# Optimization experiments

Hardware: AMD Instinct MI355X
Metric: run time of the kernel (lower is better)

## Reference

```python
import jax, jax.numpy as jnp
import numpy as np
from jax import lax

MAX_INT = 10000.0
V, T0, E, H = 100000, 20, 256, 256
T = T0 + 2          # tagset_size + 2 (start = T-2, stop = T-1)
B, S = 32, 512
H2 = H // 2


def setup_inputs() -> dict:
    key = jax.random.key(0)
    ks = jax.random.split(key, 18)
    sd = 0.08
    trans = jax.random.normal(ks[0], (T, T), jnp.float32)
    trans = trans.at[-2, :].set(-MAX_INT).at[:, -1].set(-MAX_INT)
    return {
        "X": jax.random.randint(ks[1], (B, S), 0, V, jnp.int64),
        "Y": jax.random.randint(ks[2], (B, S), 0, T0, jnp.int64),
        "emb": jax.random.normal(ks[3], (V, E), jnp.float32) * sd,
        "Wih_f": jax.random.normal(ks[4], (4 * H2, E), jnp.float32) * sd,
        "Whh_f": jax.random.normal(ks[5], (4 * H2, H2), jnp.float32) * sd,
        "bih_f": jax.random.normal(ks[6], (4 * H2,), jnp.float32) * sd,
        "bhh_f": jax.random.normal(ks[7], (4 * H2,), jnp.float32) * sd,
        "Wih_b": jax.random.normal(ks[8], (4 * H2, E), jnp.float32) * sd,
        "Whh_b": jax.random.normal(ks[9], (4 * H2, H2), jnp.float32) * sd,
        "bih_b": jax.random.normal(ks[10], (4 * H2,), jnp.float32) * sd,
        "bhh_b": jax.random.normal(ks[11], (4 * H2,), jnp.float32) * sd,
        "fcW": jax.random.normal(ks[12], (T, H), jnp.float32) * sd,
        "fcb": jax.random.normal(ks[13], (T,), jnp.float32) * sd,
        "trans": trans,
        # original draws random (h0, c0) of shape (2, seq_len, H//2) each call
        "h0": jax.random.normal(ks[14], (2, S, H2), jnp.float32),
        "c0": jax.random.normal(ks[15], (2, S, H2), jnp.float32),
    }


def _lstm_dir(x, h0, c0, Wih, Whh, bih, bhh, reverse):
    # x: [B, S, E]; scans over axis 0 (as torch LSTM with batch_first=False does here)
    def step(carry, xt):
        h, c = carry
        g = xt @ Wih.T + bih + h @ Whh.T + bhh          # [S, 4*H2]
        i, f, gg, o = jnp.split(g, 4, axis=-1)
        c2 = jax.nn.sigmoid(f) * c + jax.nn.sigmoid(i) * jnp.tanh(gg)
        h2 = jax.nn.sigmoid(o) * jnp.tanh(c2)
        return (h2, c2), h2
    xs = x[::-1] if reverse else x
    _, hs = lax.scan(step, (h0, c0), xs)
    return hs[::-1] if reverse else hs                  # [B, S, H2]


def _feats(X, emb, Wih_f, Whh_f, bih_f, bhh_f, Wih_b, Whh_b, bih_b, bhh_b,
           fcW, fcb, h0, c0):
    e = emb[X]                                           # [B, S, E]
    hf = _lstm_dir(e, h0[0], c0[0], Wih_f, Whh_f, bih_f, bhh_f, False)
    hb = _lstm_dir(e, h0[1], c0[1], Wih_b, Whh_b, bih_b, bhh_b, True)
    lstm_out = jnp.concatenate([hf, hb], axis=-1)        # [B, S, H]
    return lstm_out @ fcW.T + fcb                        # [B, S, T]


def _crf_loss(feats, Y, trans):
    # forward algorithm (log partition), vectorized over batch
    alpha0 = jnp.full((B, T), -MAX_INT, feats.dtype).at[:, -2].set(0.0)

    def step(alpha, feat_t):                             # feat_t: [B, T]
        # alpha_new[b, next] = LSE_prev(alpha[b,prev] + trans[next,prev]) + feat[b,next]
        new = jax.nn.logsumexp(alpha[:, None, :] + trans[None, :, :], axis=2) + feat_t
        return new, None

    alpha, _ = lax.scan(step, alpha0, jnp.swapaxes(feats, 0, 1))
    forward_score = jax.nn.logsumexp(alpha + trans[-1][None, :], axis=1).mean()

    # gold score
    start = jnp.full((B, 1), T - 2, Y.dtype)
    tags = jnp.concatenate([start, Y], axis=1)           # [B, S+1]
    emit = jnp.take_along_axis(feats, Y[..., None], axis=2)[..., 0].sum(axis=1)
    trans_sc = trans[tags[:, 1:], tags[:, :-1]].sum(axis=1) + trans[-1, tags[:, -1]]
    gold_score = (emit + trans_sc).mean()
    return forward_score - gold_score


def reference(X, Y, emb, Wih_f, Whh_f, bih_f, bhh_f, Wih_b, Whh_b, bih_b, bhh_b,
              fcW, fcb, trans, h0, c0):
    feats = _feats(X, emb, Wih_f, Whh_f, bih_f, bhh_f, Wih_b, Whh_b, bih_b, bhh_b,
                   fcW, fcb, h0, c0)
    score = _crf_loss(feats, Y, trans)
    return score, Y
```

## Files before the change

### kernel.cpp

```cpp
#include <hip/hip_runtime.h>
#include <hip/hip_bf16.h>
#include <stdint.h>

typedef __attribute__((ext_vector_type(8))) short short8;
typedef __attribute__((ext_vector_type(4))) float f32x4;
typedef __attribute__((ext_vector_type(4))) unsigned short ushort4v;

#define NB 32
#define NS 512
#define NE 256
#define NH2 128
#define NG 512
#define NT 22

__device__ __forceinline__ unsigned short f2bf(float f) {
    union { float f; unsigned u; } v; v.f = f;
    unsigned r = v.u + 0x7fffu + ((v.u >> 16) & 1u);
    return (unsigned short)(r >> 16);
}
__device__ __forceinline__ float bf2f(unsigned short b) {
    union { unsigned u; float f; } v; v.u = ((unsigned)b) << 16;
    return v.f;
}
__device__ __forceinline__ float sigmoidf_(float x) {
    return __builtin_amdgcn_rcpf(1.f + __expf(-x));
}
__device__ __forceinline__ float tanhf_(float x) {
    return 1.f - 2.f * __builtin_amdgcn_rcpf(__expf(2.f * x) + 1.f);
}
__device__ __forceinline__ void wg_barrier() {
    __builtin_amdgcn_sched_barrier(0);
    asm volatile("s_waitcnt lgkmcnt(0)" ::: "memory");
    __builtin_amdgcn_s_barrier();
    __builtin_amdgcn_sched_barrier(0);
}
#define GL16(gsrc, ldst)                                                              \
    __builtin_amdgcn_global_load_lds(                                                 \
        (const __attribute__((address_space(1))) unsigned int*)(gsrc),                \
        (__attribute__((address_space(3))) unsigned int*)(ldst), 16, 0, 0)

__global__ void k_pre(const int* X, const float* emb, const int* Y,
                      const float* Wih_f, const float* Wih_b,
                      const float* Whh_f, const float* Whh_b, const float* fcW,
                      unsigned short* ebf, unsigned short* Wb_ih,
                      unsigned short* Wb_hh, unsigned short* fcpad, float* out)
{
    int idx = blockIdx.x * blockDim.x + threadIdx.x;
    const int nEmb = NB * NS * 64;
    if (idx < nEmb) {
        int r = idx >> 6, lane = idx & 63;
        int xr = X[r];
        f32x4 v = *(const f32x4*)(emb + (size_t)xr * NE + lane * 4);
        ushort4v o;
        o[0] = f2bf(v[0]); o[1] = f2bf(v[1]); o[2] = f2bf(v[2]); o[3] = f2bf(v[3]);
        *(ushort4v*)(ebf + (size_t)r * NE + lane * 4) = o;
        return;
    }
    int j = idx - nEmb;
    const int n1 = 2 * NG * NE;
    const int n2 = 2 * NG * NH2;
    const int n3 = 2 * 32 * NH2;
    const int n4 = NB * NS;
    if (j < n1) {
        const float* src = (j < NG * NE) ? Wih_f : Wih_b;
        Wb_ih[j] = f2bf(src[j % (NG * NE)]);
    } else if (j < n1 + n2) {
        int i2 = j - n1;
        const float* src = (i2 < NG * NH2) ? Whh_f : Whh_b;
        Wb_hh[i2] = f2bf(src[i2 % (NG * NH2)]);
    } else if (j < n1 + n2 + n3) {
        int i3 = j - n1 - n2;
        int d = i3 / (32 * NH2);
        int jj = (i3 / NH2) % 32;
        int k = i3 % NH2;
        fcpad[i3] = (jj < NT) ? f2bf(fcW[jj * 256 + d * NH2 + k]) : (unsigned short)0;
    } else if (j < n1 + n2 + n3 + n4) {
        int i4 = j - n1 - n2 - n3;
        out[1 + i4] = (float)Y[i4];
    }
}

__launch_bounds__(256)
__global__ void k_xproj(const unsigned short* ebf, const unsigned short* Wb_ih,
                        const float* bih_f, const float* bhh_f,
                        const float* bih_b, const float* bhh_b,
                        unsigned short* Xp)
{
    __shared__ __align__(16) unsigned short Atile[2][128 * 64];
    __shared__ __align__(16) unsigned short Btile[2][128 * 64];
    int dir = blockIdx.z;
    int r0 = blockIdx.x * 128;
    int g0 = blockIdx.y * 128;
    int tid = threadIdx.x;
    int w = tid >> 6, lane = tid & 63;
    int wr = w >> 1, wc = w & 1;
    int lrow = lane & 15, kg = lane >> 4;
    int srow8 = lane >> 3, schunk = lane & 7;
    const float* bih = dir ? bih_b : bih_f;
    const float* bhh = dir ? bhh_b : bhh_f;
    const unsigned short* Bsrc = Wb_ih + ((size_t)dir * NG + g0) * NE;
    const unsigned short* Asrc = ebf + (size_t)r0 * NE;

#define STAGE(bufi, ks)                                                                \
    do {                                                                               \
        int k0_ = (ks) * 64;                                                           \
        _Pragma("unroll")                                                              \
        for (int i_ = 0; i_ < 4; ++i_) {                                               \
            int rr_ = (w * 4 + i_) * 8 + srow8;                                        \
            GL16(Asrc + (size_t)rr_ * NE + k0_ + schunk * 8, &Atile[bufi][(w * 4 + i_) * 512]); \
            GL16(Bsrc + (size_t)rr_ * NE + k0_ + schunk * 8, &Btile[bufi][(w * 4 + i_) * 512]); \
        }                                                                              \
    } while (0)

    STAGE(0, 0);
    f32x4 acc[4][4] = {};
#pragma unroll
    for (int ks = 0; ks < 4; ++ks) {
        const int cur = ks & 1;
        if (ks < 3) {
            STAGE(cur ^ 1, ks + 1);
            asm volatile("s_waitcnt vmcnt(8)" ::: "memory");
        } else {
            asm volatile("s_waitcnt vmcnt(0)" ::: "memory");
        }
        __builtin_amdgcn_sched_barrier(0);
        __builtin_amdgcn_s_barrier();
        __builtin_amdgcn_sched_barrier(0);
        short8 a[4][2], b[4][2];
#pragma unroll
        for (int mi = 0; mi < 4; ++mi)
#pragma unroll
            for (int kk = 0; kk < 2; ++kk)
                a[mi][kk] = *(const short8*)&Atile[cur][(wr * 64 + mi * 16 + lrow) * 64 + kk * 32 + kg * 8];
#pragma unroll
        for (int ni = 0; ni < 4; ++ni)
#pragma unroll
            for (int kk = 0; kk < 2; ++kk)
                b[ni][kk] = *(const short8*)&Btile[cur][(wc * 64 + ni * 16 + lrow) * 64 + kk * 32 + kg * 8];
#pragma unroll
        for (int mi = 0; mi < 4; ++mi)
#pragma unroll
            for (int ni = 0; ni < 4; ++ni)
#pragma unroll
                for (int kk = 0; kk < 2; ++kk)
                    acc[mi][ni] = __builtin_amdgcn_mfma_f32_16x16x32_bf16(a[mi][kk], b[ni][kk], acc[mi][ni], 0, 0, 0);
        asm volatile("s_waitcnt lgkmcnt(0)" ::: "memory");
        __builtin_amdgcn_sched_barrier(0);
        __builtin_amdgcn_s_barrier();
        __builtin_amdgcn_sched_barrier(0);
    }
#undef STAGE

#pragma unroll
    for (int ni = 0; ni < 4; ++ni) {
        int g = g0 + wc * 64 + ni * 16 + lrow;
        float bias = bih[g] + bhh[g];
#pragma unroll
        for (int mi = 0; mi < 4; ++mi) {
            int r = r0 + wr * 64 + mi * 16 + kg * 4;
            int t = r >> 9;
            int s = r & 511;
            int sb = s >> 4;
            unsigned short* dst = Xp + ((((size_t)dir * 32 + sb) * 32 + t) << 13) + g * 16 + (s & 15);
            unsigned o0 = f2bf(acc[mi][ni][0] + bias);
            unsigned o1 = f2bf(acc[mi][ni][1] + bias);
            unsigned o2 = f2bf(acc[mi][ni][2] + bias);
            unsigned o3 = f2bf(acc[mi][ni][3] + bias);
            uint2 pk; pk.x = o0 | (o1 << 16); pk.y = o2 | (o3 << 16);
            *(uint2*)dst = pk;
        }
    }
}

__launch_bounds__(512, 2)
__global__ void k_lstm(const unsigned short* Wb_hh, const unsigned short* fcpad,
                       const unsigned short* Xp, const float* h0, const float* c0,
                       float* featsP)
{
    __shared__ unsigned short h_lds[2][16 * 136];
    __shared__ float featsL[32 * 16 * 24];
    int dir = blockIdx.x >> 5;
    int sb = blockIdx.x & 31;
    int s0 = sb * 16;
    int tid = threadIdx.x;
    int w = tid >> 6, lane = tid & 63;
    int lrow = lane & 15, kg = lane >> 4;

    short8 bfr[4][4];
#pragma unroll
    for (int q = 0; q < 4; ++q) {
        const unsigned short* p = Wb_hh + ((size_t)dir * NG + (q * 128 + w * 16 + lrow)) * NH2 + kg * 8;
#pragma unroll
        for (int kf = 0; kf < 4; ++kf)
            bfr[q][kf] = *(const short8*)(p + kf * 32);
    }
    short8 fcfr[4];
    if (w < 2) {
        const unsigned short* p = fcpad + ((size_t)dir * 32 + (w * 16 + lrow)) * NH2 + kg * 8;
#pragma unroll
        for (int kf = 0; kf < 4; ++kf)
            fcfr[kf] = *(const short8*)(p + kf * 32);
    }

    float c[4];
#pragma unroll
    for (int i = 0; i < 4; ++i)
        c[i] = c0[((size_t)dir * NS + s0 + kg * 4 + i) * NH2 + w * 16 + lrow];
    {
        int sl = tid >> 5, hq = tid & 31;
        f32x4 hv = *(const f32x4*)(h0 + ((size_t)dir * NS + s0 + sl) * NH2 + hq * 4);
        ushort4v hb; hb[0] = f2bf(hv[0]); hb[1] = f2bf(hv[1]); hb[2] = f2bf(hv[2]); hb[3] = f2bf(hv[3]);
        *(ushort4v*)&h_lds[0][sl * 136 + hq * 4] = hb;
    }

    const unsigned short* xbase = Xp + (((size_t)dir * 32 + sb) * 32) * 8192;
    int xoff0 = (w * 16 + lrow) * 16 + kg * 4;
    ushort4v xA[4], xB[4];
#pragma unroll
    for (int q = 0; q < 4; ++q)
        xA[q] = *(const ushort4v*)(xbase + (size_t)(dir ? 31 : 0) * 8192 + xoff0 + q * 2048);
#pragma unroll
    for (int q = 0; q < 4; ++q)
        xB[q] = *(const ushort4v*)(xbase + (size_t)(dir ? 30 : 1) * 8192 + xoff0 + q * 2048);
    __syncthreads();

#define LSTM_STEP(T, XV, PR, PW)                                                       \
    {                                                                                  \
        short8 afr[4];                                                                 \
        _Pragma("unroll")                                                              \
        for (int kf = 0; kf < 4; ++kf)                                                 \
            afr[kf] = *(const short8*)&h_lds[PR][lrow * 136 + kf * 32 + kg * 8];       \
        f32x4 acc[4] = {};                                                             \
        _Pragma("unroll")                                                              \
        for (int q = 0; q < 4; ++q)                                                    \
            _Pragma("unroll")                                                          \
            for (int kf = 0; kf < 4; ++kf)                                             \
                acc[q] = __builtin_amdgcn_mfma_f32_16x16x32_bf16(afr[kf], bfr[q][kf],  \
                                                                 acc[q], 0, 0, 0);     \
        if (w < 2 && (T) > 0) {                     \
            int txp = dir ? 32 - (T) : (T) - 1;                                        \
            f32x4 fa = {};                                                             \
            _Pragma("unroll")                                                          \
            for (int kf = 0; kf < 4; ++kf)                                             \
                fa = __builtin_amdgcn_mfma_f32_16x16x32_bf16(afr[kf], fcfr[kf], fa, 0, 0, 0); \
            int tag = w * 16 + lrow;                                                   \
            if (tag < NT) {                                                            \
                _Pragma("unroll")                                                      \
                for (int i = 0; i < 4; ++i)                                            \
                    featsL[(txp * 16 + kg * 4 + i) * 24 + tag] = fa[i];                \
            }                                                                          \
        }                                                                              \
        float gs[4][4];                                                                \
        _Pragma("unroll")                                                              \
        for (int q = 0; q < 4; ++q)                                                    \
            _Pragma("unroll")                                                          \
            for (int i = 0; i < 4; ++i)                                                \
                gs[q][i] = acc[q][i] + bf2f(XV[q][i]);                                 \
        if ((T) + 2 < 32) {                                                            \
            int txn = dir ? 29 - (T) : (T) + 2;                                        \
            _Pragma("unroll")                                                          \
            for (int q = 0; q < 4; ++q)                                                \
                XV[q] = *(const ushort4v*)(xbase + (size_t)txn * 8192 + xoff0 + q * 2048); \
        }                                                                              \
        _Pragma("unroll")                                                              \
        for (int i = 0; i < 4; ++i) {                                                  \
            float ci = sigmoidf_(gs[1][i]) * c[i] + sigmoidf_(gs[0][i]) * tanhf_(gs[2][i]); \
            c[i] = ci;                                                                 \
            h_lds[PW][(kg * 4 + i) * 136 + w * 16 + lrow] = f2bf(sigmoidf_(gs[3][i]) * tanhf_(ci)); \
        }                                                                              \
        wg_barrier();                                                                  \
    }

    for (int tt = 0; tt < 16; ++tt) {
        LSTM_STEP(2 * tt,     xA, ((2 * tt) & 1),     (((2 * tt) & 1) ^ 1))
        LSTM_STEP(2 * tt + 1, xB, ((2 * tt + 1) & 1), (((2 * tt + 1) & 1) ^ 1))
    }
#undef LSTM_STEP

    if (w < 2) {
        short8 afr[4];
#pragma unroll
        for (int kf = 0; kf < 4; ++kf)
            afr[kf] = *(const short8*)&h_lds[0][lrow * 136 + kf * 32 + kg * 8];
        f32x4 fa = {};
#pragma unroll
        for (int kf = 0; kf < 4; ++kf)
            fa = __builtin_amdgcn_mfma_f32_16x16x32_bf16(afr[kf], fcfr[kf], fa, 0, 0, 0);
        int txl = dir ? 0 : 31;
        int tag = w * 16 + lrow;
        if (tag < NT) {
#pragma unroll
            for (int i = 0; i < 4; ++i)
                featsL[(txl * 16 + kg * 4 + i) * 24 + tag] = fa[i];
        }
    }
    __syncthreads();
    int ftx = tid >> 4, fs = tid & 15;
    float* gdst = featsP + (((size_t)dir * 32 + ftx) * 512 + s0 + fs) * 24;
    const float* lsrc = featsL + (ftx * 16 + fs) * 24;
#pragma unroll
    for (int j = 0; j < 6; ++j)
        ((f32x4*)gdst)[j] = ((const f32x4*)lsrc)[j];
}

__device__ __forceinline__ float mm_combine(const unsigned short* Rb, const unsigned short* Tb,
                                            int lane, f32x4 c[2][2])
{
    int lrow = lane & 15, kg = lane >> 4;
    short8 a0 = *(const short8*)(Rb + lrow * 32 + kg * 8);
    short8 a1 = *(const short8*)(Rb + (16 + lrow) * 32 + kg * 8);
    short8 b0 = *(const short8*)(Tb + lrow * 32 + kg * 8);
    short8 b1 = *(const short8*)(Tb + (16 + lrow) * 32 + kg * 8);
    c[0][0] = __builtin_amdgcn_mfma_f32_16x16x32_bf16(a0, b0, c[0][0], 0, 0, 0);
    c[0][1] = __builtin_amdgcn_mfma_f32_16x16x32_bf16(a0, b1, c[0][1], 0, 0, 0);
    c[1][0] = __builtin_amdgcn_mfma_f32_16x16x32_bf16(a1, b0, c[1][0], 0, 0, 0);
    c[1][1] = __builtin_amdgcn_mfma_f32_16x16x32_bf16(a1, b1, c[1][1], 0, 0, 0);
    float mx = 0.f;
#pragma unroll
    for (int ti = 0; ti < 2; ++ti)
#pragma unroll
        for (int tj = 0; tj < 2; ++tj)
#pragma unroll
            for (int i = 0; i < 4; ++i) mx = fmaxf(mx, c[ti][tj][i]);
#pragma unroll
    for (int off = 32; off; off >>= 1) mx = fmaxf(mx, __shfl_xor(mx, off));
    return fmaxf(mx, 1e-30f);
}

__device__ __forceinline__ void write_scaled(unsigned short* outp, bool Rlayout,
                                             int lane, const f32x4 c[2][2], float inv)
{
    int lrow = lane & 15, kg = lane >> 4;
    if (Rlayout) {
#pragma unroll
        for (int ti = 0; ti < 2; ++ti)
#pragma unroll
            for (int tj = 0; tj < 2; ++tj) {
                int cc = tj * 16 + lrow;
#pragma unroll
                for (int i = 0; i < 4; ++i) {
                    int r = ti * 16 + kg * 4 + i;
                    float v = (r < NT && cc < NT) ? c[ti][tj][i] * inv : 0.f;
                    outp[r * 32 + cc] = f2bf(v);
                }
            }
    } else {
#pragma unroll
        for (int ti = 0; ti < 2; ++ti)
#pragma unroll
            for (int tj = 0; tj < 2; ++tj) {
                int cc = tj * 16 + lrow;
                int r0 = ti * 16 + kg * 4;
                ushort4v pk;
#pragma unroll
                for (int i = 0; i < 4; ++i) {
                    int r = r0 + i;
                    float v = (r < NT && cc < NT) ? c[ti][tj][i] * inv : 0.f;
                    pk[i] = f2bf(v);
                }
                *(ushort4v*)(outp + cc * 32 + r0) = pk;
            }
    }
}

__launch_bounds__(256)
__global__ void k_fcrf(const float* featsP, const float* fcb, const float* trans,
                       const int* Y, unsigned short* Mseg, float* lscseg, float* goldp)
{
    __shared__ unsigned short mats[16 * 1024];
    __shared__ float etR[484], etT[484];
    __shared__ float ef[16 * 24];
    __shared__ float fl[16 * 24];
    __shared__ float lscm[16];
    int b = blockIdx.x, seg = blockIdx.y;
    int tid = threadIdx.x;
    int w = tid >> 6, lane = tid & 63;

    for (int i = tid; i < 484; i += 256) {
        float e = __expf(trans[i]);
        etR[i] = e;
        etT[(i % NT) * NT + (i / NT)] = e;
    }
    for (int i = tid; i < 16 * NT; i += 256) {
        int s = i / NT, j = i % NT;
        size_t base = ((size_t)b * 512 + seg * 16 + s) * 24 + j;
        float f = featsP[base] + featsP[(size_t)32 * 512 * 24 + base] + fcb[j];
        fl[s * 24 + j] = f;
        ef[s * 24 + j] = __expf(f);
    }
    if (tid < 16) lscm[tid] = 0.f;
    __syncthreads();

    if (w == 3 && lane < 16) {
        int sg = seg * 16 + lane;
        int y = Y[b * NS + sg];
        int yp = sg ? Y[b * NS + sg - 1] : (NT - 2);
        float gp = fl[lane * 24 + y] + trans[y * NT + yp];
#pragma unroll
        for (int off = 8; off; off >>= 1) gp += __shfl_xor(gp, off);
        if (lane == 0) goldp[b * 32 + seg] = gp;
    }

    for (int idx = tid; idx < 16 * 1024; idx += 256) {
        int t = idx >> 10, cell = idx & 1023, row = cell >> 5, col = cell & 31;
        float v = 0.f;
        if (row < NT && col < NT) {
            v = (t & 1) ? etR[row * NT + col] * ef[t * 24 + row]
                        : etT[row * NT + col] * ef[t * 24 + col];
        }
        mats[idx] = f2bf(v);
    }
    __syncthreads();

    for (int lvl = 0; lvl < 4; ++lvl) {
        int nP = 8 >> lvl;
        for (int p = w; p < nP; p += 4) {
            int aslot = (2 * p) << lvl, bslot = (2 * p + 1) << lvl;
            f32x4 c[2][2] = {};
            float mx = mm_combine(mats + bslot * 1024, mats + aslot * 1024, lane, c);
            float inv = __builtin_amdgcn_rcpf(mx);
            float nlsc = lscm[aslot] + lscm[bslot] + __logf(mx);
            if (lvl < 3) {
                write_scaled(mats + aslot * 1024, (p & 1) != 0, lane, c, inv);
                if (lane == 0) lscm[aslot] = nlsc;
            } else {
                write_scaled(Mseg + ((size_t)b * 32 + seg) * 1024, (seg & 1) != 0, lane, c, inv);
                if (lane == 0) lscseg[b * 32 + seg] = nlsc;
            }
        }
        __syncthreads();
    }
}

__launch_bounds__(256)
__global__ void k_crf2(const unsigned short* Mseg, const float* lscseg,
                       const float* trans, const int* Y, const float* goldp,
                       float* fwd_sc, float* gold_sc)
{
    __shared__ unsigned short mats[16 * 1024];
    __shared__ float lscm[16];
    __shared__ float tl[484];
    __shared__ float col20[32];
    int b = blockIdx.x;
    int tid = threadIdx.x;
    int w = tid >> 6, lane = tid & 63;
    int lrow = lane & 15, kg = lane >> 4;

    for (int i = tid; i < 484; i += 256) tl[i] = trans[i];
    __syncthreads();

    const unsigned short* base = Mseg + (size_t)b * 32 * 1024;
    for (int p = w; p < 16; p += 4) {
        f32x4 c[2][2] = {};
        float mx = mm_combine(base + (2 * p + 1) * 1024, base + (2 * p) * 1024, lane, c);
        float inv = __builtin_amdgcn_rcpf(mx);
        float nlsc = lscseg[b * 32 + 2 * p] + lscseg[b * 32 + 2 * p + 1] + __logf(mx);
        write_scaled(mats + p * 1024, (p & 1) != 0, lane, c, inv);
        if (lane == 0) lscm[p] = nlsc;
    }
    __syncthreads();

    for (int lvl = 0; lvl < 4; ++lvl) {
        int nP = 8 >> lvl;
        for (int p = w; p < nP; p += 4) {
            int aslot = (2 * p) << lvl, bslot = (2 * p + 1) << lvl;
            f32x4 c[2][2] = {};
            float mx = mm_combine(mats + bslot * 1024, mats + aslot * 1024, lane, c);
            if (lvl < 3) {
                float inv = __builtin_amdgcn_rcpf(mx);
                float nlsc = lscm[aslot] + lscm[bslot] + __logf(mx);
                write_scaled(mats + aslot * 1024, (p & 1) != 0, lane, c, inv);
                if (lane == 0) lscm[aslot] = nlsc;
            } else {
                if (lrow == 4) {
#pragma unroll
                    for (int ti = 0; ti < 2; ++ti)
#pragma unroll
                        for (int i = 0; i < 4; ++i)
                            col20[ti * 16 + kg * 4 + i] = c[ti][1][i];
                }
                if (lane == 0) lscm[0] = lscm[0] + lscm[8];
            }
        }
        __syncthreads();
    }

    if (w == 0) {
        float v = 0.f;
        if (lane < NT) v = __expf(tl[(NT - 1) * NT + lane]) * col20[lane];
#pragma unroll
        for (int off = 32; off; off >>= 1) v += __shfl_xor(v, off);
        if (lane == 0) fwd_sc[b] = __logf(v) + lscm[0];
    }
    if (w == 1) {
        float g = (lane < 32) ? goldp[b * 32 + lane] : 0.f;
#pragma unroll
        for (int off = 16; off; off >>= 1) g += __shfl_xor(g, off);
        if (lane == 0) gold_sc[b] = g + tl[(NT - 1) * NT + Y[b * NS + NS - 1]];
    }
}

__global__ void k_final(const float* fwd_sc, const float* gold_sc, float* out)
{
    float v = (threadIdx.x < NB) ? (fwd_sc[threadIdx.x] - gold_sc[threadIdx.x]) : 0.f;
#pragma unroll
    for (int off = 32; off; off >>= 1) v += __shfl_xor(v, off);
    if (threadIdx.x == 0) out[0] = v * (1.f / NB);
}

extern "C" void kernel_launch(void* const* d_in, const int* in_sizes, int n_in,
                              void* d_out, int out_size, void* d_ws, size_t ws_size,
                              hipStream_t stream)
{
    const int* X = (const int*)d_in[0];
    const int* Y = (const int*)d_in[1];
    const float* emb = (const float*)d_in[2];
    const float* Wih_f = (const float*)d_in[3];
    const float* Whh_f = (const float*)d_in[4];
    const float* bih_f = (const float*)d_in[5];
    const float* bhh_f = (const float*)d_in[6];
    const float* Wih_b = (const float*)d_in[7];
    const float* Whh_b = (const float*)d_in[8];
    const float* bih_b = (const float*)d_in[9];
    const float* bhh_b = (const float*)d_in[10];
    const float* fcW = (const float*)d_in[11];
    const float* fcb = (const float*)d_in[12];
    const float* trans = (const float*)d_in[13];
    const float* h0 = (const float*)d_in[14];
    const float* c0 = (const float*)d_in[15];
    float* out = (float*)d_out;

    char* ws = (char*)d_ws;
    unsigned short* Wb_ih = (unsigned short*)(ws + 0);
    unsigned short* Wb_hh = (unsigned short*)(ws + 524288);
    unsigned short* fcpad = (unsigned short*)(ws + 786432);
    unsigned short* Xp    = (unsigned short*)(ws + 802816);
    float* featsP         = (float*)(ws + 34357248);
    float* goldp          = (float*)(ws + 37502976);
    float* fwd_sc         = (float*)(ws + 37507072);
    float* gold_sc        = (float*)(ws + 37507200);
    unsigned short* ebf   = (unsigned short*)(ws + 37507328);
    unsigned short* Mseg  = ebf;
    float* lscseg         = (float*)(ws + 45895936);

    k_pre<<<dim3(5728), dim3(256), 0, stream>>>(X, emb, Y, Wih_f, Wih_b, Whh_f, Whh_b,
                                                fcW, ebf, Wb_ih, Wb_hh, fcpad, out);
    k_xproj<<<dim3(128, 4, 2), dim3(256), 0, stream>>>(ebf, Wb_ih, bih_f, bhh_f, bih_b, bhh_b, Xp);
    k_lstm<<<dim3(64), dim3(512), 0, stream>>>(Wb_hh, fcpad, Xp, h0, c0, featsP);
    k_fcrf<<<dim3(32, 32), dim3(256), 0, stream>>>(featsP, fcb, trans, Y, Mseg, lscseg, goldp);
    k_crf2<<<dim3(NB), dim3(256), 0, stream>>>(Mseg, lscseg, trans, Y, goldp, fwd_sc, gold_sc);
    k_final<<<dim3(1), dim3(64), 0, stream>>>(fwd_sc, gold_sc, out);
    (void)in_sizes; (void)n_in; (void)out_size; (void)ws_size;
}
```

Baseline: 97.98 us.

## Shorten LSTM recurrence critical path and spread FC projection across waves

Restructures the per-step LSTM recurrence. The x-projection now seeds the MFMA accumulator, and the K reduction is split into two independent accumulator chains to cut dependent MFMA latency. The gate math is merged so fewer reciprocals are needed, and h is packed to bf16 with a hardware convert. The FC feature projection is spread across all 8 waves as partial products in LDS and reduced one step late, instead of two waves doing a serial 4-MFMA chain. Features are stored as bf16, which halves the intermediate traffic at some cost in precision.

```diff
diff --git a/kernel.cpp b/kernel.cpp
--- a/kernel.cpp
+++ b/kernel.cpp
@@ -5,6 +5,7 @@
 typedef __attribute__((ext_vector_type(8))) short short8;
 typedef __attribute__((ext_vector_type(4))) float f32x4;
 typedef __attribute__((ext_vector_type(4))) unsigned short ushort4v;
+typedef __attribute__((ext_vector_type(4))) unsigned int uint4v;
 
 #define NB 32
 #define NS 512
@@ -22,11 +23,10 @@
     union { unsigned u; float f; } v; v.u = ((unsigned)b) << 16;
     return v.f;
 }
-__device__ __forceinline__ float sigmoidf_(float x) {
-    return __builtin_amdgcn_rcpf(1.f + __expf(-x));
-}
-__device__ __forceinline__ float tanhf_(float x) {
-    return 1.f - 2.f * __builtin_amdgcn_rcpf(__expf(2.f * x) + 1.f);
+__device__ __forceinline__ unsigned cvt_pk_bf16(float a, float b) {
+    unsigned r;
+    asm("v_cvt_pk_bf16_f32 %0, %1, %2" : "=v"(r) : "v"(a), "v"(b));
+    return r;
 }
 __device__ __forceinline__ void wg_barrier() {
     __builtin_amdgcn_sched_barrier(0);
@@ -175,10 +175,11 @@
 __launch_bounds__(512, 2)
 __global__ void k_lstm(const unsigned short* Wb_hh, const unsigned short* fcpad,
                        const unsigned short* Xp, const float* h0, const float* c0,
-                       float* featsP)
+                       unsigned short* featsP)
 {
     __shared__ unsigned short h_lds[2][16 * 136];
-    __shared__ float featsL[32 * 16 * 24];
+    __shared__ unsigned short featsL[512 * 24];
+    __shared__ f32x4 fcpart[2][8][64];
     int dir = blockIdx.x >> 5;
     int sb = blockIdx.x & 31;
     int s0 = sb * 16;
@@ -194,13 +195,8 @@
         for (int kf = 0; kf < 4; ++kf)
             bfr[q][kf] = *(const short8*)(p + kf * 32);
     }
-    short8 fcfr[4];
-    if (w < 2) {
-        const unsigned short* p = fcpad + ((size_t)dir * 32 + (w * 16 + lrow)) * NH2 + kg * 8;
-#pragma unroll
-        for (int kf = 0; kf < 4; ++kf)
-            fcfr[kf] = *(const short8*)(p + kf * 32);
-    }
+    short8 fcfr8 = *(const short8*)(fcpad + ((size_t)dir * 32 + ((w >> 2) * 16 + lrow)) * NH2 + (w & 3) * 32 + kg * 8);
+    int fctag = (w >> 2) * 16 + lrow;
 
     float c[4];
 #pragma unroll
@@ -224,38 +220,50 @@
         xB[q] = *(const ushort4v*)(xbase + (size_t)(dir ? 30 : 1) * 8192 + xoff0 + q * 2048);
     __syncthreads();
 
+#define FC_REDUCE(par, hstep)                                                          \
+    if (w < 2) {                                                                       \
+        int txp_ = dir ? 31 - (hstep) : (hstep);                                       \
+        f32x4 fa_ = fcpart[par][w * 4 + 0][lane] + fcpart[par][w * 4 + 1][lane]        \
+                  + fcpart[par][w * 4 + 2][lane] + fcpart[par][w * 4 + 3][lane];       \
+        int tag_ = w * 16 + lrow;                                                      \
+        if (tag_ < NT) {                                                               \
+            unsigned r01_ = cvt_pk_bf16(fa_[0], fa_[1]);                               \
+            unsigned r23_ = cvt_pk_bf16(fa_[2], fa_[3]);                               \
+            int rb_ = (txp_ * 16 + kg * 4) * 24 + tag_;                                \
+            featsL[rb_]      = (unsigned short)r01_;                                   \
+            featsL[rb_ + 24] = (unsigned short)(r01_ >> 16);                           \
+            featsL[rb_ + 48] = (unsigned short)r23_;                                   \
+            featsL[rb_ + 72] = (unsigned short)(r23_ >> 16);                           \
+        }                                                                              \
+    }
+
 #define LSTM_STEP(T, XV, PR, PW)                                                       \
     {                                                                                  \
         short8 afr[4];                                                                 \
         _Pragma("unroll")                                                              \
         for (int kf = 0; kf < 4; ++kf)                                                 \
             afr[kf] = *(const short8*)&h_lds[PR][lrow * 136 + kf * 32 + kg * 8];       \
-        f32x4 acc[4] = {};                                                             \
+        f32x4 accA[4], accB[4];                                                        \
         _Pragma("unroll")                                                              \
-        for (int q = 0; q < 4; ++q)                                                    \
-            _Pragma("unroll")                                                          \
-            for (int kf = 0; kf < 4; ++kf)                                             \
-                acc[q] = __builtin_amdgcn_mfma_f32_16x16x32_bf16(afr[kf], bfr[q][kf],  \
-                                                                 acc[q], 0, 0, 0);     \
-        if (w < 2 && (T) > 0) {                     \
-            int txp = dir ? 32 - (T) : (T) - 1;                                        \
-            f32x4 fa = {};                                                             \
-            _Pragma("unroll")                                                          \
-            for (int kf = 0; kf < 4; ++kf)                                             \
-                fa = __builtin_amdgcn_mfma_f32_16x16x32_bf16(afr[kf], fcfr[kf], fa, 0, 0, 0); \
-            int tag = w * 16 + lrow;                                                   \
-            if (tag < NT) {                                                            \
-                _Pragma("unroll")                                                      \
-                for (int i = 0; i < 4; ++i)                                            \
-                    featsL[(txp * 16 + kg * 4 + i) * 24 + tag] = fa[i];                \
-            }                                                                          \
-        }                                                                              \
-        float gs[4][4];                                                                \
+        for (int q = 0; q < 4; ++q) {                                                  \
+            f32x4 ci_;                                                                 \
+            ci_[0] = bf2f(XV[q][0]); ci_[1] = bf2f(XV[q][1]);                          \
+            ci_[2] = bf2f(XV[q][2]); ci_[3] = bf2f(XV[q][3]);                          \
+            accA[q] = __builtin_amdgcn_mfma_f32_16x16x32_bf16(afr[0], bfr[q][0], ci_, 0, 0, 0); \
+            f32x4 z_ = {};                                                             \
+            accB[q] = __builtin_amdgcn_mfma_f32_16x16x32_bf16(afr[2], bfr[q][2], z_, 0, 0, 0);  \
+        }                                                                              \
         _Pragma("unroll")                                                              \
-        for (int q = 0; q < 4; ++q)                                                    \
-            _Pragma("unroll")                                                          \
-            for (int i = 0; i < 4; ++i)                                                \
-                gs[q][i] = acc[q][i] + bf2f(XV[q][i]);                                 \
+        for (int q = 0; q < 4; ++q) {                                                  \
+            accA[q] = __builtin_amdgcn_mfma_f32_16x16x32_bf16(afr[1], bfr[q][1], accA[q], 0, 0, 0); \
+            accB[q] = __builtin_amdgcn_mfma_f32_16x16x32_bf16(afr[3], bfr[q][3], accB[q], 0, 0, 0); \
+        }                                                                              \
+        {         \
+            f32x4 z_ = {};                                                             \
+            f32x4 fp_ = __builtin_amdgcn_mfma_f32_16x16x32_bf16(afr[w & 3], fcfr8, z_, 0, 0, 0); \
+            fcpart[(T) & 1][w][lane] = fp_;                                            \
+        }                                                                              \
+        if ((T) >= 2) { FC_REDUCE(((T) - 1) & 1, (T) - 2) }                            \
         if ((T) + 2 < 32) {                                                            \
             int txn = dir ? 29 - (T) : (T) + 2;                                        \
             _Pragma("unroll")                                                          \
@@ -264,43 +272,65 @@
         }                                                                              \
         _Pragma("unroll")                                                              \
         for (int i = 0; i < 4; ++i) {                                                  \
-            float ci = sigmoidf_(gs[1][i]) * c[i] + sigmoidf_(gs[0][i]) * tanhf_(gs[2][i]); \
-            c[i] = ci;                                                                 \
-            h_lds[PW][(kg * 4 + i) * 136 + w * 16 + lrow] = f2bf(sigmoidf_(gs[3][i]) * tanhf_(ci)); \
+            float gi_ = accA[0][i] + accB[0][i];                                       \
+            float gf_ = accA[1][i] + accB[1][i];                                       \
+            float gg_ = accA[2][i] + accB[2][i];                                       \
+            float go_ = accA[3][i] + accB[3][i];                                       \
+            float ef_ = __expf(-gf_);                                                  \
+            float sfc_ = c[i] * __builtin_amdgcn_rcpf(1.f + ef_);                      \
+            float eg2_ = __expf(2.f * gg_);                                            \
+            float ei_ = __expf(-gi_);                                                  \
+            float tgsi_ = (eg2_ - 1.f) * __builtin_amdgcn_rcpf((1.f + ei_) * (eg2_ + 1.f)); \
+            float cn_ = sfc_ + tgsi_;                                                  \
+            c[i] = cn_;                                                                \
+            float ec2_ = __expf(2.f * cn_);                                            \
+            float eo_ = __expf(-go_);                                                  \
+            c[i + 4] = (ec2_ - 1.f) * __builtin_amdgcn_rcpf((1.f + eo_) * (ec2_ + 1.f)); \
+        }                                                                              \
+        {                                                                              \
+            unsigned r01_ = cvt_pk_bf16(c[4], c[5]);                                   \
+            unsigned r23_ = cvt_pk_bf16(c[6], c[7]);                                   \
+            int hb_ = (kg * 4) * 136 + w * 16 + lrow;                                  \
+            h_lds[PW][hb_]           = (unsigned short)r01_;                           \
+            h_lds[PW][hb_ + 136]     = (unsigned short)(r01_ >> 16);                   \
+            h_lds[PW][hb_ + 272]     = (unsigned short)r23_;                           \
+            h_lds[PW][hb_ + 408]     = (unsigned short)(r23_ >> 16);                   \
         }                                                                              \
         wg_barrier();                                                                  \
     }
 
-    for (int tt = 0; tt < 16; ++tt) {
-        LSTM_STEP(2 * tt,     xA, ((2 * tt) & 1),     (((2 * tt) & 1) ^ 1))
-        LSTM_STEP(2 * tt + 1, xB, ((2 * tt + 1) & 1), (((2 * tt + 1) & 1) ^ 1))
+    float cfull[8];
+#pragma unroll
+    for (int i = 0; i < 4; ++i) cfull[i] = c[i];
+    {
+#define c cfull
+        for (int tt = 0; tt < 16; ++tt) {
+            LSTM_STEP(2 * tt,     xA, ((2 * tt) & 1),     (((2 * tt) & 1) ^ 1))
+            LSTM_STEP(2 * tt + 1, xB, ((2 * tt + 1) & 1), (((2 * tt + 1) & 1) ^ 1))
+        }
+#undef c
     }
 #undef LSTM_STEP
 
-    if (w < 2) {
-        short8 afr[4];
-#pragma unroll
-        for (int kf = 0; kf < 4; ++kf)
-            afr[kf] = *(const short8*)&h_lds[0][lrow * 136 + kf * 32 + kg * 8];
-        f32x4 fa = {};
-#pragma unroll
-        for (int kf = 0; kf < 4; ++kf)
-            fa = __builtin_amdgcn_mfma_f32_16x16x32_bf16(afr[kf], fcfr[kf], fa, 0, 0, 0);
-        int txl = dir ? 0 : 31;
-        int tag = w * 16 + lrow;
-        if (tag < NT) {
-#pragma unroll
-            for (int i = 0; i < 4; ++i)
-                featsL[(txl * 16 + kg * 4 + i) * 24 + tag] = fa[i];
-        }
-    }
+    FC_REDUCE(1, 30)
+    {
+        short8 a2 = *(const short8*)&h_lds[0][lrow * 136 + (w & 3) * 32 + kg * 8];
+        f32x4 z_ = {};
+        f32x4 fp_ = __builtin_amdgcn_mfma_f32_16x16x32_bf16(a2, fcfr8, z_, 0, 0, 0);
+        fcpart[0][w][lane] = fp_;
+    }
+    wg_barrier();
+    FC_REDUCE(0, 31)
     __syncthreads();
+    (void)fctag;
+
     int ftx = tid >> 4, fs = tid & 15;
-    float* gdst = featsP + (((size_t)dir * 32 + ftx) * 512 + s0 + fs) * 24;
-    const float* lsrc = featsL + (ftx * 16 + fs) * 24;
-#pragma unroll
-    for (int j = 0; j < 6; ++j)
-        ((f32x4*)gdst)[j] = ((const f32x4*)lsrc)[j];
+    unsigned short* gdst = featsP + (((size_t)dir * 32 + ftx) * 512 + s0 + fs) * 24;
+    const unsigned short* lsrc = featsL + (ftx * 16 + fs) * 24;
+#pragma unroll
+    for (int j = 0; j < 3; ++j)
+        ((uint4v*)gdst)[j] = ((const uint4v*)lsrc)[j];
+#undef FC_REDUCE
 }
 
 __device__ __forceinline__ float mm_combine(const unsigned short* Rb, const unsigned short* Tb,
@@ -364,7 +394,7 @@
 }
 
 __launch_bounds__(256)
-__global__ void k_fcrf(const float* featsP, const float* fcb, const float* trans,
+__global__ void k_fcrf(const unsigned short* featsP, const float* fcb, const float* trans,
                        const int* Y, unsigned short* Mseg, float* lscseg, float* goldp)
 {
     __shared__ unsigned short mats[16 * 1024];
@@ -384,7 +414,7 @@
     for (int i = tid; i < 16 * NT; i += 256) {
         int s = i / NT, j = i % NT;
         size_t base = ((size_t)b * 512 + seg * 16 + s) * 24 + j;
-        float f = featsP[base] + featsP[(size_t)32 * 512 * 24 + base] + fcb[j];
+        float f = bf2f(featsP[base]) + bf2f(featsP[(size_t)32 * 512 * 24 + base]) + fcb[j];
         fl[s * 24 + j] = f;
         ef[s * 24 + j] = __expf(f);
     }
@@ -531,17 +561,17 @@
     float* out = (float*)d_out;
 
     char* ws = (char*)d_ws;
-    unsigned short* Wb_ih = (unsigned short*)(ws + 0);
-    unsigned short* Wb_hh = (unsigned short*)(ws + 524288);
-    unsigned short* fcpad = (unsigned short*)(ws + 786432);
-    unsigned short* Xp    = (unsigned short*)(ws + 802816);
-    float* featsP         = (float*)(ws + 34357248);
-    float* goldp          = (float*)(ws + 37502976);
-    float* fwd_sc         = (float*)(ws + 37507072);
-    float* gold_sc        = (float*)(ws + 37507200);
-    unsigned short* ebf   = (unsigned short*)(ws + 37507328);
-    unsigned short* Mseg  = ebf;
-    float* lscseg         = (float*)(ws + 45895936);
+    unsigned short* Wb_ih  = (unsigned short*)(ws + 0);
+    unsigned short* Wb_hh  = (unsigned short*)(ws + 524288);
+    unsigned short* fcpad  = (unsigned short*)(ws + 786432);
+    unsigned short* Xp     = (unsigned short*)(ws + 802816);
+    unsigned short* featsP = (unsigned short*)(ws + 34357248);
+    float* goldp           = (float*)(ws + 35930112);
+    float* fwd_sc          = (float*)(ws + 35934208);
+    float* gold_sc         = (float*)(ws + 35934336);
+    unsigned short* ebf    = (unsigned short*)(ws + 35934464);
+    unsigned short* Mseg   = ebf;
+    float* lscseg          = (float*)(ws + 44323072);
 
     k_pre<<<dim3(5728), dim3(256), 0, stream>>>(X, emb, Y, Wih_f, Wih_b, Whh_f, Whh_b,
                                                 fcW, ebf, Wb_ih, Wb_hh, fcpad, out);
```

Result: slower. 149.9 us (+52.9%).
